# Kernel optimization log

Hardware: AMD Instinct MI355X
Metric: run time of the kernel (lower is better)

Reference implementation:

```python
import jax, jax.numpy as jnp
import numpy as np

N_ATOMS = 100000
IN_F = 512
HID = 512
OUT_F = 256
N_SPECIES = 64
EMB_DIM = 16
N_ROUTED = 6
N_SHARED = 2
TOPK = 2


def setup_inputs() -> dict:
    key = jax.random.key(0)
    ks = jax.random.split(key, 12)
    s = 0.02
    return {
        "features": jax.random.normal(ks[0], (N_ATOMS, IN_F), dtype=jnp.float32),
        "species_idx": jax.random.randint(ks[1], (N_ATOMS,), 0, N_SPECIES),
        "emb": jax.random.normal(ks[2], (N_SPECIES, EMB_DIM), dtype=jnp.float32),
        "W_router": jax.random.normal(ks[3], (N_ROUTED, EMB_DIM), dtype=jnp.float32) * s,
        "rW1": jax.random.normal(ks[4], (N_ROUTED, HID, IN_F), dtype=jnp.float32) * s,
        "rb1": jax.random.normal(ks[5], (N_ROUTED, HID), dtype=jnp.float32) * s,
        "rW2": jax.random.normal(ks[6], (N_ROUTED, OUT_F, HID), dtype=jnp.float32) * s,
        "rb2": jax.random.normal(ks[7], (N_ROUTED, OUT_F), dtype=jnp.float32) * s,
        "sW1": jax.random.normal(ks[8], (N_SHARED, HID, IN_F), dtype=jnp.float32) * s,
        "sb1": jax.random.normal(ks[9], (N_SHARED, HID), dtype=jnp.float32) * s,
        "sW2": jax.random.normal(ks[10], (N_SHARED, OUT_F, HID), dtype=jnp.float32) * s,
        "sb2": jax.random.normal(ks[11], (N_SHARED, OUT_F), dtype=jnp.float32) * s,
    }


def _expert_mlp(x, W1, b1, W2, b2):
    # x: [n, d]; W1: [E, h, d]; W2: [E, o, h] -> [n, E, o]
    h = jax.nn.silu(jnp.einsum("nd,ehd->neh", x, W1) + b1)
    return jnp.einsum("neh,eoh->neo", h, W2) + b2


def reference(features, species_idx, emb, W_router, rW1, rb1, rW2, rb2, sW1, sb1, sW2, sb2):
    # Router: u = SiLU(Embedding(z)); scores = softmax(W_e u)
    u = jax.nn.silu(emb[species_idx])                    # [n, M]
    scores = jax.nn.softmax(u @ W_router.T, axis=-1)     # [n, I]
    topk_scores, topk_idx = jax.lax.top_k(scores, TOPK)
    n = scores.shape[0]
    routing_weights = jnp.zeros_like(scores).at[
        jnp.arange(n)[:, None], topk_idx
    ].set(topk_scores)                                   # sparse gates [n, I]

    routed = _expert_mlp(features, rW1, rb1, rW2, rb2)   # [n, I, o]
    out = jnp.einsum("ne,neo->no", routing_weights, routed)

    shared = _expert_mlp(features, sW1, sb1, sW2, sb2)   # [n, S, o]
    return out + shared.sum(axis=1)
```

## Files before the change

kernel.cpp:

```cpp
#include <hip/hip_runtime.h>
#include <hip/hip_bf16.h>


typedef __attribute__((ext_vector_type(8))) short short8;
typedef __attribute__((ext_vector_type(4))) float f32x4;

#define IN_F 512
#define HID  512
#define OUT_F 256
#define TILE 64

__device__ inline unsigned short f2bf(float f) {
    __hip_bfloat16 h = __float2bfloat16(f);
    return *reinterpret_cast<unsigned short*>(&h);
}

__device__ __forceinline__ void dma16(const unsigned short* g, unsigned short* l) {
    __builtin_amdgcn_global_load_lds(
        (const __attribute__((address_space(1))) unsigned int*)(unsigned long long)(const void*)g,
        (__attribute__((address_space(3))) unsigned int*)(unsigned int)(unsigned long long)(void*)l,
        16, 0, 0);
}

__device__ __forceinline__ void stage_chunk(const unsigned short* gbase,
                                            unsigned short* lbase,
                                            int w, int lane) {
    dma16(gbase + w * 1024 +       lane * 8, lbase + w * 1024);
    dma16(gbase + w * 1024 + 512 + lane * 8, lbase + w * 1024 + 512);
}

__global__ void k_cvt_w1(const float* __restrict__ rW1, const float* __restrict__ sW1,
                         unsigned short* __restrict__ dst) {
    int i = blockIdx.x * 256 + threadIdx.x;
    int col = i & 31;
    int row = (i >> 5) & 255;
    int kq  = (i >> 13) & 15;
    int j   = (i >> 17) & 1;
    int ex  = i >> 18;
    int hrow = j * 256 + row;
    int kcol = kq * 32 + col;
    float v = (ex < 6) ? rW1[((size_t)ex * 512 + hrow) * 512 + kcol]
                       : sW1[((size_t)(ex - 6) * 512 + hrow) * 512 + kcol];
    dst[i] = f2bf(v);
}

__global__ void k_cvt_w2(const float* __restrict__ rW2, const float* __restrict__ sW2,
                         unsigned short* __restrict__ dst) {
    int i = blockIdx.x * 256 + threadIdx.x;
    int col = i & 31;
    int row = (i >> 5) & 255;
    int kq  = (i >> 13) & 7;
    int j   = (i >> 16) & 1;
    int ex  = i >> 17;
    int kcol = j * 256 + kq * 32 + col;
    float v = (ex < 6) ? rW2[((size_t)ex * 256 + row) * 512 + kcol]
                       : sW2[((size_t)(ex - 6) * 256 + row) * 512 + kcol];
    dst[i] = f2bf(v);
}

__global__ void k_fill(int* __restrict__ counts, int* __restrict__ cursors,
                       int* __restrict__ idxl, int* __restrict__ tile_pair,
                       int CAP, int TMAX) {
    int i = blockIdx.x * 256 + threadIdx.x;
    if (i < 16) { counts[i] = 0; cursors[i] = 0; }
    if (i < TMAX) tile_pair[i] = -1;
    if (i < CAP) idxl[i] = -1;
}

__global__ void k_router(const int* __restrict__ species, const float* __restrict__ emb,
                         const float* __restrict__ Wr,
                         int* __restrict__ pid, float* __restrict__ gA, float* __restrict__ gB,
                         int* __restrict__ counts, int N) {
    __shared__ int lcnt[16];
    int tid = threadIdx.x;
    if (tid < 16) lcnt[tid] = 0;
    __syncthreads();
    int i = blockIdx.x * 256 + tid;
    if (i < N) {
        int z = species[i];
        float u[16];
#pragma unroll
        for (int k = 0; k < 16; ++k) {
            float v = emb[z * 16 + k];
            u[k] = v / (1.f + __expf(-v));
        }
        float s[6];
        float mx = -1e30f;
#pragma unroll
        for (int e = 0; e < 6; ++e) {
            float a = 0.f;
#pragma unroll
            for (int k = 0; k < 16; ++k) a += u[k] * Wr[e * 16 + k];
            s[e] = a;
            mx = fmaxf(mx, a);
        }
        float sum = 0.f;
#pragma unroll
        for (int e = 0; e < 6; ++e) { s[e] = __expf(s[e] - mx); sum += s[e]; }
        float inv = 1.f / sum;
        int i0 = 0;
#pragma unroll
        for (int e = 1; e < 6; ++e) if (s[e] > s[i0]) i0 = e;
        int i1 = (i0 == 0) ? 1 : 0;
#pragma unroll
        for (int e = 0; e < 6; ++e) if (e != i0 && s[e] > s[i1]) i1 = e;
        float g0 = s[i0] * inv, g1 = s[i1] * inv;
        int a = min(i0, i1), b = max(i0, i1);
        const int PB[5] = {0, 5, 9, 12, 14};
        int p = PB[a] + (b - a - 1);
        pid[i] = p;
        gA[i] = (a == i0) ? g0 : g1;
        gB[i] = (a == i0) ? g1 : g0;
        atomicAdd(&lcnt[p], 1);
    }
    __syncthreads();
    if (tid < 15 && lcnt[tid] > 0) atomicAdd(&counts[tid], lcnt[tid]);
}

__global__ void k_scan(const int* __restrict__ counts, int* __restrict__ offs,
                       int* __restrict__ tile_pair, int TMAX) {
    __shared__ int so[16];
    if (threadIdx.x == 0) {
        int acc = 0;
        for (int p = 0; p < 15; ++p) { so[p] = acc; acc += (counts[p] + 63) & ~63; }
        so[15] = acc;
        for (int p = 0; p < 16; ++p) offs[p] = so[p];
    }
    __syncthreads();
    for (int t = threadIdx.x; t < TMAX; t += blockDim.x) {
        int t64 = t * 64;
        if (t64 < so[15]) {
            int p = 0;
            while (!(t64 >= so[p] && t64 < so[p + 1])) ++p;
            tile_pair[t] = p;
        }
    }
}

__global__ void k_scatter(const int* __restrict__ pid, const float* __restrict__ gA,
                          const float* __restrict__ gB, const int* __restrict__ offs,
                          int* __restrict__ cursors, int* __restrict__ idxl,
                          float* __restrict__ gAl, float* __restrict__ gBl, int N) {
    __shared__ int lcnt[16], lbase[16];
    int tid = threadIdx.x;
    if (tid < 16) lcnt[tid] = 0;
    __syncthreads();
    int i = blockIdx.x * 256 + tid;
    int p = -1, rank = 0;
    if (i < N) { p = pid[i]; rank = atomicAdd(&lcnt[p], 1); }
    __syncthreads();
    if (tid < 15 && lcnt[tid] > 0) lbase[tid] = atomicAdd(&cursors[tid], lcnt[tid]);
    __syncthreads();
    if (i < N) {
        int slot = offs[p] + lbase[p] + rank;
        idxl[slot] = i; gAl[slot] = gA[i]; gBl[slot] = gB[i];
    }
}

__global__ __launch_bounds__(512, 2) void k_moe(
    const float* __restrict__ X,
    const unsigned short* __restrict__ W1pk,
    const unsigned short* __restrict__ W2pk,
    const int* __restrict__ idxl, const float* __restrict__ gAl,
    const float* __restrict__ gBl, const int* __restrict__ tile_pair,
    const float* __restrict__ rb1, const float* __restrict__ rb2,
    const float* __restrict__ sb1, const float* __restrict__ sb2,
    float* __restrict__ Y)
{
    int t;
    {
        const int nwg = (int)gridDim.x;
        const int q = nwg >> 3, r = nwg & 7;
        const int xcd = (int)blockIdx.x & 7;
        const int idx = (int)blockIdx.x >> 3;
        t = (xcd < r ? xcd * (q + 1) : r * (q + 1) + (xcd - r) * q) + idx;
    }
    const int p = tile_pair[t];
    if (p < 0) return;
    int ea = 0, eb = 1;
    {
        int pp = p;
#pragma unroll
        for (int a = 0; a < 5; ++a) {
            int span = 5 - a;
            if (pp < span) { ea = a; eb = a + 1 + pp; break; }
            pp -= span;
        }
    }

    __shared__ __align__(16) unsigned short xs[TILE][520];
    __shared__ __align__(16) unsigned short hs[TILE][264];
    __shared__ __align__(16) unsigned short wlds[2][8192];
    __shared__ float gsA[TILE], gsB[TILE];
    __shared__ int idxs[TILE];

    const int tid = threadIdx.x;
    if (tid < TILE) {
        int slot = t * TILE + tid;
        int gi = idxl[slot];
        idxs[tid] = gi;
        gsA[tid] = (gi >= 0) ? gAl[slot] : 0.f;
        gsB[tid] = (gi >= 0) ? gBl[slot] : 0.f;
    }
    __syncthreads();

    for (int i = tid; i < TILE * 128; i += 512) {
        int r = i >> 7, c4 = i & 127;
        int gi = idxs[r]; if (gi < 0) gi = 0;
        f32x4 v = __builtin_nontemporal_load(
            reinterpret_cast<const f32x4*>(X + (size_t)gi * IN_F) + c4);
        ushort4 pk;
        pk.x = f2bf(v.x); pk.y = f2bf(v.y); pk.z = f2bf(v.z); pk.w = f2bf(v.w);
        *reinterpret_cast<ushort4*>(&xs[r][c4 * 4]) = pk;
    }

    const int w    = tid >> 6;
    const int lane = tid & 63;
    const int mw   = w >> 2;
    const int nw   = w & 3;
    const int quad = lane >> 4;
    const int l16  = lane & 15;

    f32x4 outacc[2][4] = {};

    for (int ei = 0; ei < 4; ++ei) {
        const int ex = (ei == 0) ? ea : (ei == 1) ? eb : (ei + 4);
        const float* b1 = (ex < 6) ? rb1 + ex * HID   : sb1 + (ex - 6) * HID;
        const float* b2 = (ex < 6) ? rb2 + ex * OUT_F : sb2 + (ex - 6) * OUT_F;

        float gr[8];
#pragma unroll
        for (int mt = 0; mt < 2; ++mt)
#pragma unroll
            for (int r = 0; r < 4; ++r) {
                int row = mw * 32 + mt * 16 + quad * 4 + r;
                gr[mt * 4 + r] = (ei == 0) ? gsA[row] : (ei == 1) ? gsB[row] : 1.f;
            }

        for (int j = 0; j < 2; ++j) {
            const unsigned short* w1c = W1pk + ((size_t)ex * 2 + j) * (16 * 8192);
            stage_chunk(w1c, wlds[0], w, lane);
            __syncthreads();

            f32x4 acc[2][4] = {};
#pragma unroll
            for (int kq = 0; kq < 16; ++kq) {
                const unsigned short* cur = wlds[kq & 1];
                if (kq + 1 < 16)
                    stage_chunk(w1c + (kq + 1) * 8192, wlds[(kq + 1) & 1], w, lane);
                short8 b[4], a[2];
#pragma unroll
                for (int nt = 0; nt < 4; ++nt)
                    b[nt] = *reinterpret_cast<const short8*>(
                        cur + (nw * 64 + nt * 16 + l16) * 32 + quad * 8);
#pragma unroll
                for (int mt = 0; mt < 2; ++mt)
                    a[mt] = *reinterpret_cast<const short8*>(
                        &xs[mw * 32 + mt * 16 + l16][kq * 32 + quad * 8]);
#pragma unroll
                for (int mt = 0; mt < 2; ++mt)
#pragma unroll
                    for (int nt = 0; nt < 4; ++nt)
                        acc[mt][nt] = __builtin_amdgcn_mfma_f32_16x16x32_bf16(
                            a[mt], b[nt], acc[mt][nt], 0, 0, 0);
                __syncthreads();
            }

#pragma unroll
            for (int mt = 0; mt < 2; ++mt)
#pragma unroll
                for (int nt = 0; nt < 4; ++nt) {
                    int hcol = nw * 64 + nt * 16 + l16;
                    float bb = b1[j * 256 + hcol];
#pragma unroll
                    for (int r = 0; r < 4; ++r) {
                        int row = mw * 32 + mt * 16 + quad * 4 + r;
                        float v = acc[mt][nt][r] + bb;
                        float h = v / (1.f + __expf(-v));
                        hs[row][hcol] = f2bf(h * gr[mt * 4 + r]);
                    }
                }

            const unsigned short* w2c = W2pk + ((size_t)ex * 2 + j) * (8 * 8192);
            stage_chunk(w2c, wlds[0], w, lane);
            __syncthreads();

#pragma unroll
            for (int kq = 0; kq < 8; ++kq) {
                const unsigned short* cur = wlds[kq & 1];
                if (kq + 1 < 8)
                    stage_chunk(w2c + (kq + 1) * 8192, wlds[(kq + 1) & 1], w, lane);
                short8 b[4], a[2];
#pragma unroll
                for (int nt = 0; nt < 4; ++nt)
                    b[nt] = *reinterpret_cast<const short8*>(
                        cur + (nw * 64 + nt * 16 + l16) * 32 + quad * 8);
#pragma unroll
                for (int mt = 0; mt < 2; ++mt)
                    a[mt] = *reinterpret_cast<const short8*>(
                        &hs[mw * 32 + mt * 16 + l16][kq * 32 + quad * 8]);
#pragma unroll
                for (int mt = 0; mt < 2; ++mt)
#pragma unroll
                    for (int nt = 0; nt < 4; ++nt)
                        outacc[mt][nt] = __builtin_amdgcn_mfma_f32_16x16x32_bf16(
                            a[mt], b[nt], outacc[mt][nt], 0, 0, 0);
                __syncthreads();
            }
        }

#pragma unroll
        for (int mt = 0; mt < 2; ++mt)
#pragma unroll
            for (int nt = 0; nt < 4; ++nt) {
                float bb = b2[nw * 64 + nt * 16 + l16];
#pragma unroll
                for (int r = 0; r < 4; ++r)
                    outacc[mt][nt][r] += gr[mt * 4 + r] * bb;
            }
    }

#pragma unroll
    for (int mt = 0; mt < 2; ++mt)
#pragma unroll
        for (int nt = 0; nt < 4; ++nt)
#pragma unroll
            for (int r = 0; r < 4; ++r) {
                int row = mw * 32 + mt * 16 + quad * 4 + r;
                int gi = idxs[row];
                if (gi >= 0)
                    __builtin_nontemporal_store(outacc[mt][nt][r],
                        Y + (size_t)gi * OUT_F + nw * 64 + nt * 16 + l16);
            }
}

extern "C" void kernel_launch(void* const* d_in, const int* in_sizes, int n_in,
                              void* d_out, int out_size, void* d_ws, size_t ws_size,
                              hipStream_t stream) {
    const float* X       = (const float*)d_in[0];
    const int*   species = (const int*)d_in[1];
    const float* emb     = (const float*)d_in[2];
    const float* Wr      = (const float*)d_in[3];
    const float* rW1     = (const float*)d_in[4];
    const float* rb1     = (const float*)d_in[5];
    const float* rW2     = (const float*)d_in[6];
    const float* rb2     = (const float*)d_in[7];
    const float* sW1     = (const float*)d_in[8];
    const float* sb1     = (const float*)d_in[9];
    const float* sW2     = (const float*)d_in[10];
    const float* sb2     = (const float*)d_in[11];
    float* Y = (float*)d_out;
    const int N = in_sizes[1];

    const int TMAX = (N + 15 * 64 + 63) / 64;
    const int CAP  = TMAX * 64;

    size_t o = 0;
    auto take = [&](size_t bytes) { size_t r = o; o += (bytes + 255) & ~(size_t)255; return r; };
    char* ws = (char*)d_ws;
    unsigned short* w1bf   = (unsigned short*)(ws + take((size_t)8 * HID * IN_F * 2));
    unsigned short* w2bf   = (unsigned short*)(ws + take((size_t)8 * OUT_F * HID * 2));
    int*   pid      = (int*)  (ws + take((size_t)N * 4));
    float* gA       = (float*)(ws + take((size_t)N * 4));
    float* gB       = (float*)(ws + take((size_t)N * 4));
    int*   counts   = (int*)  (ws + take(64));
    int*   cursors  = (int*)  (ws + take(64));
    int*   offs     = (int*)  (ws + take(64));
    int*   idxl     = (int*)  (ws + take((size_t)CAP * 4));
    float* gAl      = (float*)(ws + take((size_t)CAP * 4));
    float* gBl      = (float*)(ws + take((size_t)CAP * 4));
    int*   tile_pair= (int*)  (ws + take((size_t)TMAX * 4));

    k_cvt_w1<<<(8 * HID * IN_F) / 256, 256, 0, stream>>>(rW1, sW1, w1bf);
    k_cvt_w2<<<(8 * OUT_F * HID) / 256, 256, 0, stream>>>(rW2, sW2, w2bf);
    k_fill<<<(CAP + 255) / 256, 256, 0, stream>>>(counts, cursors, idxl, tile_pair, CAP, TMAX);
    k_router<<<(N + 255) / 256, 256, 0, stream>>>(species, emb, Wr, pid, gA, gB, counts, N);
    k_scan<<<1, 256, 0, stream>>>(counts, offs, tile_pair, TMAX);
    k_scatter<<<(N + 255) / 256, 256, 0, stream>>>(pid, gA, gB, offs, cursors, idxl, gAl, gBl, N);
    k_moe<<<TMAX, 512, 0, stream>>>(X, w1bf, w2bf, idxl, gAl, gBl, tile_pair,
                                    rb1, rb2, sb1, sb2, Y);
}
```

Measured before the change: 1.002 ms.

## Triple-buffer weight chunks with one barrier per step and swizzled LDS layout

Replaces the double-buffered weight staging, which used two __syncthreads per chunk, with a three-slot ring buffer. Each step uses one s_barrier guarded by explicit vmcnt/lgkmcnt waits, and the DMA runs two chunks ahead. The W1 stream now prefetches the first W2 chunks across the GEMM1/GEMM2 boundary. Weight packing is XOR-swizzled so MFMA B-operand reads from LDS avoid bank conflicts. This uses more LDS per block, which could lower occupancy, and relies on hand-placed waitcnt for correctness (e.g. the hs writes before GEMM2 are only covered by the barrier at c=16).

```diff
diff --git a/kernel.cpp b/kernel.cpp
--- a/kernel.cpp
+++ b/kernel.cpp
@@ -9,6 +9,11 @@
 #define HID  512
 #define OUT_F 256
 #define TILE 64
+#define CH   8192
+
+#define WAIT_LGKM0 asm volatile("s_waitcnt lgkmcnt(0)" ::: "memory")
+#define WAIT_VM2   asm volatile("s_waitcnt vmcnt(2)"   ::: "memory")
+#define WAIT_VM0   asm volatile("s_waitcnt vmcnt(0)"   ::: "memory")
 
 __device__ inline unsigned short f2bf(float f) {
     __hip_bfloat16 h = __float2bfloat16(f);
@@ -22,21 +27,22 @@
         16, 0, 0);
 }
 
-__device__ __forceinline__ void stage_chunk(const unsigned short* gbase,
-                                            unsigned short* lbase,
-                                            int w, int lane) {
-    dma16(gbase + w * 1024 +       lane * 8, lbase + w * 1024);
-    dma16(gbase + w * 1024 + 512 + lane * 8, lbase + w * 1024 + 512);
+__device__ __forceinline__ void stage_chunk(const unsigned short* g,
+                                            unsigned short* l, int w, int lane) {
+    dma16(g + w * 1024 +       lane * 8, l + w * 1024);
+    dma16(g + w * 1024 + 512 + lane * 8, l + w * 1024 + 512);
 }
 
 __global__ void k_cvt_w1(const float* __restrict__ rW1, const float* __restrict__ sW1,
                          unsigned short* __restrict__ dst) {
     int i = blockIdx.x * 256 + threadIdx.x;
-    int col = i & 31;
-    int row = (i >> 5) & 255;
-    int kq  = (i >> 13) & 15;
-    int j   = (i >> 17) & 1;
-    int ex  = i >> 18;
+    int low3 = i & 7;
+    int sw   = (i >> 3) & 3;
+    int row  = (i >> 5) & 255;
+    int kq   = (i >> 13) & 15;
+    int j    = (i >> 17) & 1;
+    int ex   = i >> 18;
+    int col  = ((sw ^ ((row >> 1) & 3)) << 3) + low3;
     int hrow = j * 256 + row;
     int kcol = kq * 32 + col;
     float v = (ex < 6) ? rW1[((size_t)ex * 512 + hrow) * 512 + kcol]
@@ -47,11 +53,13 @@
 __global__ void k_cvt_w2(const float* __restrict__ rW2, const float* __restrict__ sW2,
                          unsigned short* __restrict__ dst) {
     int i = blockIdx.x * 256 + threadIdx.x;
-    int col = i & 31;
-    int row = (i >> 5) & 255;
-    int kq  = (i >> 13) & 7;
-    int j   = (i >> 16) & 1;
-    int ex  = i >> 17;
+    int low3 = i & 7;
+    int sw   = (i >> 3) & 3;
+    int row  = (i >> 5) & 255;
+    int kq   = (i >> 13) & 7;
+    int j    = (i >> 16) & 1;
+    int ex   = i >> 17;
+    int col  = ((sw ^ ((row >> 1) & 3)) << 3) + low3;
     int kcol = j * 256 + kq * 32 + col;
     float v = (ex < 6) ? rW2[((size_t)ex * 256 + row) * 512 + kcol]
                        : sW2[((size_t)(ex - 6) * 256 + row) * 512 + kcol];
@@ -190,7 +198,7 @@
 
     __shared__ __align__(16) unsigned short xs[TILE][520];
     __shared__ __align__(16) unsigned short hs[TILE][264];
-    __shared__ __align__(16) unsigned short wlds[2][8192];
+    __shared__ __align__(16) unsigned short wlds[3][CH];
     __shared__ float gsA[TILE], gsB[TILE];
     __shared__ int idxs[TILE];
 
@@ -213,6 +221,7 @@
         pk.x = f2bf(v.x); pk.y = f2bf(v.y); pk.z = f2bf(v.z); pk.w = f2bf(v.w);
         *reinterpret_cast<ushort4*>(&xs[r][c4 * 4]) = pk;
     }
+    WAIT_VM0;
 
     const int w    = tid >> 6;
     const int lane = tid & 63;
@@ -220,6 +229,8 @@
     const int nw   = w & 3;
     const int quad = lane >> 4;
     const int l16  = lane & 15;
+    const int swz  = ((quad ^ ((l16 >> 1) & 3)) << 3);
+    const int wrow = (nw * 64 + l16) * 32;
 
     f32x4 outacc[2][4] = {};
 
@@ -238,32 +249,38 @@
             }
 
         for (int j = 0; j < 2; ++j) {
-            const unsigned short* w1c = W1pk + ((size_t)ex * 2 + j) * (16 * 8192);
-            stage_chunk(w1c, wlds[0], w, lane);
-            __syncthreads();
+            const unsigned short* w1c = W1pk + ((size_t)ex * 2 + j) * (16 * CH);
+            const unsigned short* w2c = W2pk + ((size_t)ex * 2 + j) * (8 * CH);
+
+            stage_chunk(w1c,      wlds[0], w, lane);
+            stage_chunk(w1c + CH, wlds[1], w, lane);
 
             f32x4 acc[2][4] = {};
-#pragma unroll
-            for (int kq = 0; kq < 16; ++kq) {
-                const unsigned short* cur = wlds[kq & 1];
-                if (kq + 1 < 16)
-                    stage_chunk(w1c + (kq + 1) * 8192, wlds[(kq + 1) & 1], w, lane);
+
+#pragma unroll
+            for (int c = 0; c < 16; ++c) {
+                WAIT_LGKM0;
+                WAIT_VM2;
+                __builtin_amdgcn_s_barrier();
+                if (c + 2 < 16)
+                    stage_chunk(w1c + (c + 2) * CH, wlds[(c + 2) % 3], w, lane);
+                else
+                    stage_chunk(w2c + (c + 2 - 16) * CH, wlds[(c + 2) % 3], w, lane);
+                const unsigned short* cur = wlds[c % 3];
                 short8 b[4], a[2];
 #pragma unroll
                 for (int nt = 0; nt < 4; ++nt)
-                    b[nt] = *reinterpret_cast<const short8*>(
-                        cur + (nw * 64 + nt * 16 + l16) * 32 + quad * 8);
+                    b[nt] = *reinterpret_cast<const short8*>(cur + wrow + nt * 512 + swz);
 #pragma unroll
                 for (int mt = 0; mt < 2; ++mt)
                     a[mt] = *reinterpret_cast<const short8*>(
-                        &xs[mw * 32 + mt * 16 + l16][kq * 32 + quad * 8]);
+                        &xs[mw * 32 + mt * 16 + l16][c * 32 + quad * 8]);
 #pragma unroll
                 for (int mt = 0; mt < 2; ++mt)
 #pragma unroll
                     for (int nt = 0; nt < 4; ++nt)
                         acc[mt][nt] = __builtin_amdgcn_mfma_f32_16x16x32_bf16(
                             a[mt], b[nt], acc[mt][nt], 0, 0, 0);
-                __syncthreads();
             }
 
 #pragma unroll
@@ -281,31 +298,28 @@
                     }
                 }
 
-            const unsigned short* w2c = W2pk + ((size_t)ex * 2 + j) * (8 * 8192);
-            stage_chunk(w2c, wlds[0], w, lane);
-            __syncthreads();
-
-#pragma unroll
-            for (int kq = 0; kq < 8; ++kq) {
-                const unsigned short* cur = wlds[kq & 1];
-                if (kq + 1 < 8)
-                    stage_chunk(w2c + (kq + 1) * 8192, wlds[(kq + 1) & 1], w, lane);
+#pragma unroll
+            for (int c = 16; c < 24; ++c) {
+                WAIT_LGKM0;
+                if (c < 23) { WAIT_VM2; } else { WAIT_VM0; }
+                __builtin_amdgcn_s_barrier();
+                if (c + 2 < 24)
+                    stage_chunk(w2c + (c + 2 - 16) * CH, wlds[(c + 2) % 3], w, lane);
+                const unsigned short* cur = wlds[c % 3];
                 short8 b[4], a[2];
 #pragma unroll
                 for (int nt = 0; nt < 4; ++nt)
-                    b[nt] = *reinterpret_cast<const short8*>(
-                        cur + (nw * 64 + nt * 16 + l16) * 32 + quad * 8);
+                    b[nt] = *reinterpret_cast<const short8*>(cur + wrow + nt * 512 + swz);
 #pragma unroll
                 for (int mt = 0; mt < 2; ++mt)
                     a[mt] = *reinterpret_cast<const short8*>(
-                        &hs[mw * 32 + mt * 16 + l16][kq * 32 + quad * 8]);
+                        &hs[mw * 32 + mt * 16 + l16][(c - 16) * 32 + quad * 8]);
 #pragma unroll
                 for (int mt = 0; mt < 2; ++mt)
 #pragma unroll
                     for (int nt = 0; nt < 4; ++nt)
                         outacc[mt][nt] = __builtin_amdgcn_mfma_f32_16x16x32_bf16(
                             a[mt], b[nt], outacc[mt][nt], 0, 0, 0);
-                __syncthreads();
             }
         }
 
```

New measurement: 839.9 us. 1.19x faster.
